# Performance work log

Hardware: AMD Instinct MI355X
Metric: run time of the kernel (lower is better)

The kernel has to match this reference:

```python
import jax, jax.numpy as jnp
import numpy as np

BATCH = 4096
NUM_FEATURES = 2048
DEPTH = 4
KERNEL = 2
THRESHOLD = 0.0


def setup_inputs() -> dict:
    key = jax.random.key(0)
    keys = jax.random.split(key, 2 + 2 * DEPTH + 2)
    inp = {}
    inp['x'] = jax.random.normal(keys[0], (BATCH, NUM_FEATURES), dtype=jnp.float32)
    # Conv2d(1,1,kernel_size=2) weight (k,k) and scalar bias, PyTorch-style init scale
    fan_in = KERNEL * KERNEL
    bound = 1.0 / np.sqrt(fan_in)
    inp['conv_w'] = jax.random.uniform(keys[1], (KERNEL, KERNEL), jnp.float32, -bound, bound)
    inp['conv_b'] = jax.random.uniform(keys[2], (), jnp.float32, -bound, bound)
    # MLP hidden layers
    lb = 1.0 / np.sqrt(NUM_FEATURES)
    for i in range(DEPTH):
        inp[f'W{i}'] = jax.random.uniform(keys[3 + 2 * i], (NUM_FEATURES, NUM_FEATURES), jnp.float32, -lb, lb)
        inp[f'b{i}'] = jax.random.uniform(keys[4 + 2 * i], (NUM_FEATURES,), jnp.float32, -lb, lb)
    inp['Wh'] = jax.random.uniform(keys[3 + 2 * DEPTH], (2, NUM_FEATURES), jnp.float32, -lb, lb)
    inp['bh'] = jax.random.uniform(keys[4 + 2 * DEPTH], (2,), jnp.float32, -lb, lb)
    return inp


def reference(x, conv_w, conv_b, W0, b0, W1, b1, W2, b2, W3, b3, Wh, bh):
    # Per-feature ConvFilter on a constant k x k patch of value x_i collapses to
    # sigmoid(x_i * sum(conv_w) + conv_b - threshold)  -- one fused elementwise op.
    h = jax.nn.sigmoid(x * jnp.sum(conv_w) + conv_b - THRESHOLD)  # (B, F)
    for W, b in ((W0, b0), (W1, b1), (W2, b2), (W3, b3)):
        h = jax.nn.relu(h @ W.T + b)
    return h @ Wh.T + bh  # (B, 2)
```

## Files before the change

### kernel.cpp

```cpp
#include <hip/hip_runtime.h>
#include <math.h>

#define BATCH 4096
#define NF    2048

typedef signed char    i8;
typedef unsigned int   u32;
typedef __attribute__((ext_vector_type(4))) int   intx4;
typedef __attribute__((ext_vector_type(4))) float floatx4;

#define LBW 0.022097086912079612f
#define QMAX 32512.0f
#define AMAX_H 3.0f

__global__ __launch_bounds__(256) void prep_kernel(
    const float* __restrict__ x, const float* __restrict__ cw,
    const float* __restrict__ cb,
    const float* __restrict__ w0, const float* __restrict__ w1,
    const float* __restrict__ w2, const float* __restrict__ w3,
    i8* __restrict__ h1o, i8* __restrict__ h2o,
    i8* __restrict__ q1,  i8* __restrict__ q2)
{
    const int bid = blockIdx.x;
    if (bid < 8192) {
        const float s = cw[0] + cw[1] + cw[2] + cw[3];
        const float c = cb[0];
        const int i = bid * 256 + threadIdx.x;
        float4 v = ((const float4*)x)[i];
        float vv[4] = {v.x, v.y, v.z, v.w};
        char4 c1, c2;
        #pragma unroll
        for (int j = 0; j < 4; ++j) {
            float r = 1.0f / (1.0f + expf(-(vv[j] * s + c)));
            int X = (int)(r * QMAX + 0.5f);
            int h1 = (X + 128) >> 8;
            int h2 = X - (h1 << 8);
            ((i8*)&c1)[j] = (i8)h1;
            ((i8*)&c2)[j] = (i8)h2;
        }
        *(char4*)&h1o[(size_t)i * 4] = c1;
        *(char4*)&h2o[(size_t)i * 4] = c2;
    } else {
        const int b2    = bid - 8192;
        const int layer = b2 >> 12;
        const int i     = (b2 & 4095) * 256 + threadIdx.x;
        const float* w = (layer == 0) ? w0 : (layer == 1) ? w1
                       : (layer == 2) ? w2 : w3;
        const size_t base = (size_t)layer * (size_t)NF * NF;
        float4 v = ((const float4*)w)[i];
        float vv[4] = {v.x, v.y, v.z, v.w};
        char4 c1, c2;
        #pragma unroll
        for (int j = 0; j < 4; ++j) {
            int X = (int)floorf(vv[j] * (QMAX / LBW) + 0.5f);
            X = max(-32512, min(32512, X));
            int h1 = (X + 128) >> 8;
            int h2 = X - (h1 << 8);
            ((i8*)&c1)[j] = (i8)h1;
            ((i8*)&c2)[j] = (i8)h2;
        }
        *(char4*)&q1[base + (size_t)i * 4] = c1;
        *(char4*)&q2[base + (size_t)i * 4] = c2;
    }
}

#define BM 128
#define BN 128
#define BK 64

__device__ __forceinline__ void stage16(const void* g, void* l) {
    __builtin_amdgcn_global_load_lds(
        (const __attribute__((address_space(1))) u32*)g,
        (__attribute__((address_space(3))) u32*)l, 16, 0, 0);
}

__global__ __launch_bounds__(256, 2) void gemm_i8_split(
    const i8* __restrict__ A1, const i8* __restrict__ A2,
    const i8* __restrict__ B1, const i8* __restrict__ B2,
    const float* __restrict__ bias,
    i8* __restrict__ C1, i8* __restrict__ C2,
    const float* __restrict__ Wh, const float* __restrict__ bh,
    float* __restrict__ outp,
    float combo, float outscale, int last, int M, int N, int K)
{
    __shared__ i8 sA1[BM * BK];
    __shared__ i8 sA2[BM * BK];
    __shared__ i8 sB1[BN * BK];
    __shared__ i8 sB2[BN * BK];

    const int t    = threadIdx.x;
    const int wv   = t >> 6;
    const int ln   = t & 63;
    const int quad = ln >> 4;
    const int ml   = ln & 15;
    const int wm   = wv >> 1;
    const int wn   = wv & 1;
    const int bm   = blockIdx.y * BM;
    const int bn   = blockIdx.x * BN;

    const int c0 = wv * 2, c1i = wv * 2 + 1;
    int offA0 = (bm + c0 * 16 + ml) * K + quad * 16;
    int offA1 = (bm + c1i * 16 + ml) * K + quad * 16;
    int offB0 = (bn + c0 * 16 + ml) * K + quad * 16;
    int offB1 = (bn + c1i * 16 + ml) * K + quad * 16;

    intx4 zero = {0, 0, 0, 0};
    intx4 acc11[4][4], accX[4][4];
    #pragma unroll
    for (int i = 0; i < 4; ++i)
        #pragma unroll
        for (int j = 0; j < 4; ++j) { acc11[i][j] = zero; accX[i][j] = zero; }

    for (int k0 = 0; k0 < K; k0 += BK) {
        stage16(A1 + offA0, &sA1[c0 * 1024]);
        stage16(A1 + offA1, &sA1[c1i * 1024]);
        stage16(A2 + offA0, &sA2[c0 * 1024]);
        stage16(A2 + offA1, &sA2[c1i * 1024]);
        stage16(B1 + offB0, &sB1[c0 * 1024]);
        stage16(B1 + offB1, &sB1[c1i * 1024]);
        stage16(B2 + offB0, &sB2[c0 * 1024]);
        stage16(B2 + offB1, &sB2[c1i * 1024]);
        offA0 += BK; offA1 += BK; offB0 += BK; offB1 += BK;
        __syncthreads();

        intx4 a1[4], a2[4];
        #pragma unroll
        for (int i = 0; i < 4; ++i) {
            const int ca = (wm * 4 + i) * 1024 + quad * 256 + ml * 16;
            a1[i] = *(const intx4*)&sA1[ca];
            a2[i] = *(const intx4*)&sA2[ca];
        }
        #pragma unroll
        for (int j = 0; j < 4; ++j) {
            const int cb = (wn * 4 + j) * 1024 + quad * 256 + ml * 16;
            intx4 b1 = *(const intx4*)&sB1[cb];
            intx4 b2 = *(const intx4*)&sB2[cb];
            #pragma unroll
            for (int i = 0; i < 4; ++i) {
                acc11[i][j] = __builtin_amdgcn_mfma_i32_16x16x64_i8(a1[i], b1, acc11[i][j], 0, 0, 0);
                accX[i][j]  = __builtin_amdgcn_mfma_i32_16x16x64_i8(a1[i], b2, accX[i][j], 0, 0, 0);
                accX[i][j]  = __builtin_amdgcn_mfma_i32_16x16x64_i8(a2[i], b1, accX[i][j], 0, 0, 0);
            }
        }
        __syncthreads();
    }

    if (!last) {
        #pragma unroll
        for (int j = 0; j < 4; ++j) {
            const int n  = bn + wn * 64 + j * 16 + ml;
            const float bv = bias[n];
            #pragma unroll
            for (int i = 0; i < 4; ++i) {
                #pragma unroll
                for (int r = 0; r < 4; ++r) {
                    const int m = bm + wm * 64 + i * 16 + quad * 4 + r;
                    float v = fmaf(65536.0f, (float)acc11[i][j][r],
                                   256.0f * (float)accX[i][j][r]) * combo + bv;
                    v = fmaxf(v, 0.0f);
                    int X = (int)(fminf(v * outscale, QMAX) + 0.5f);
                    int h1 = (X + 128) >> 8;
                    int h2 = X - (h1 << 8);
                    C1[(size_t)m * N + n] = (i8)h1;
                    C2[(size_t)m * N + n] = (i8)h2;
                }
            }
        }
    } else {
        float wh0[4], wh1[4], bv[4];
        #pragma unroll
        for (int j = 0; j < 4; ++j) {
            const int n = bn + wn * 64 + j * 16 + ml;
            bv[j]  = bias[n];
            wh0[j] = Wh[n];
            wh1[j] = Wh[NF + n];
        }
        #pragma unroll
        for (int i = 0; i < 4; ++i) {
            #pragma unroll
            for (int r = 0; r < 4; ++r) {
                float s0 = 0.0f, s1 = 0.0f;
                #pragma unroll
                for (int j = 0; j < 4; ++j) {
                    float v = fmaf(65536.0f, (float)acc11[i][j][r],
                                   256.0f * (float)accX[i][j][r]) * combo + bv[j];
                    v = fmaxf(v, 0.0f);
                    s0 = fmaf(v, wh0[j], s0);
                    s1 = fmaf(v, wh1[j], s1);
                }
                #pragma unroll
                for (int off = 8; off > 0; off >>= 1) {
                    s0 += __shfl_xor(s0, off, 64);
                    s1 += __shfl_xor(s1, off, 64);
                }
                if (ml == 0) {
                    const int m = bm + wm * 64 + i * 16 + quad * 4 + r;
                    if (bn == 0 && wn == 0) { s0 += bh[0]; s1 += bh[1]; }
                    atomicAdd(&outp[(size_t)m * 2 + 0], s0);
                    atomicAdd(&outp[(size_t)m * 2 + 1], s1);
                }
            }
        }
    }
}

__global__ __launch_bounds__(256) void act_kernel_f32(
    const float* __restrict__ x, const float* __restrict__ conv_w,
    const float* __restrict__ conv_b, float* __restrict__ h, int n4)
{
    const float s = conv_w[0] + conv_w[1] + conv_w[2] + conv_w[3];
    const float c = conv_b[0];
    int i = blockIdx.x * blockDim.x + threadIdx.x;
    if (i < n4) {
        float4 v = ((const float4*)x)[i];
        float4 r;
        r.x = 1.0f / (1.0f + expf(-(v.x * s + c)));
        r.y = 1.0f / (1.0f + expf(-(v.y * s + c)));
        r.z = 1.0f / (1.0f + expf(-(v.z * s + c)));
        r.w = 1.0f / (1.0f + expf(-(v.w * s + c)));
        ((float4*)h)[i] = r;
    }
}

#define FBM 128
#define FBN 128
#define FBK 16
#define FPAD 4

__global__ __launch_bounds__(256) void gemm_bias_relu_f32(
    const float* __restrict__ A, const float* __restrict__ W,
    const float* __restrict__ bias, float* __restrict__ C,
    int M, int N, int K, int do_relu)
{
    __shared__ float As[FBK][FBM + FPAD];
    __shared__ float Bs[FBK][FBN + FPAD];
    const int t  = threadIdx.x;
    const int bm = blockIdx.y * FBM;
    const int bn = blockIdx.x * FBN;
    const int tn = (t & 15) * 8;
    const int tm = (t >> 4) * 8;
    const int r0 = t >> 2;
    const int kv = (t & 3) << 2;
    float acc[8][8] = {};
    for (int k0 = 0; k0 < K; k0 += FBK) {
        #pragma unroll
        for (int half = 0; half < 2; ++half) {
            const int row = r0 + half * 64;
            float4 av = *(const float4*)&A[(size_t)(bm + row) * K + k0 + kv];
            As[kv + 0][row] = av.x; As[kv + 1][row] = av.y;
            As[kv + 2][row] = av.z; As[kv + 3][row] = av.w;
            float4 bv = *(const float4*)&W[(size_t)(bn + row) * K + k0 + kv];
            Bs[kv + 0][row] = bv.x; Bs[kv + 1][row] = bv.y;
            Bs[kv + 2][row] = bv.z; Bs[kv + 3][row] = bv.w;
        }
        __syncthreads();
        #pragma unroll
        for (int kk = 0; kk < FBK; ++kk) {
            float a[8], b[8];
            *(float4*)&a[0] = *(const float4*)&As[kk][tm];
            *(float4*)&a[4] = *(const float4*)&As[kk][tm + 4];
            *(float4*)&b[0] = *(const float4*)&Bs[kk][tn];
            *(float4*)&b[4] = *(const float4*)&Bs[kk][tn + 4];
            #pragma unroll
            for (int i = 0; i < 8; ++i)
                #pragma unroll
                for (int j = 0; j < 8; ++j)
                    acc[i][j] = fmaf(a[i], b[j], acc[i][j]);
        }
        __syncthreads();
    }
    #pragma unroll
    for (int i = 0; i < 8; ++i) {
        const int row = bm + tm + i;
        #pragma unroll
        for (int j = 0; j < 8; j += 4) {
            float4 v;
            v.x = acc[i][j + 0] + bias[bn + tn + j + 0];
            v.y = acc[i][j + 1] + bias[bn + tn + j + 1];
            v.z = acc[i][j + 2] + bias[bn + tn + j + 2];
            v.w = acc[i][j + 3] + bias[bn + tn + j + 3];
            if (do_relu) {
                v.x = fmaxf(v.x, 0.0f); v.y = fmaxf(v.y, 0.0f);
                v.z = fmaxf(v.z, 0.0f); v.w = fmaxf(v.w, 0.0f);
            }
            *(float4*)&C[(size_t)row * N + bn + tn + j] = v;
        }
    }
}

__global__ __launch_bounds__(256) void head_kernel_f32(
    const float* __restrict__ h, const float* __restrict__ Wh,
    const float* __restrict__ bh, float* __restrict__ out)
{
    const int wave = threadIdx.x >> 6;
    const int lane = threadIdx.x & 63;
    const int row  = blockIdx.x * 4 + wave;
    const float* hr = h + (size_t)row * NF;
    float acc0 = 0.0f, acc1 = 0.0f;
    for (int k = lane * 4; k < NF; k += 256) {
        float4 v  = *(const float4*)&hr[k];
        float4 w0 = *(const float4*)&Wh[k];
        float4 w1 = *(const float4*)&Wh[NF + k];
        acc0 += v.x * w0.x + v.y * w0.y + v.z * w0.z + v.w * w0.w;
        acc1 += v.x * w1.x + v.y * w1.y + v.z * w1.z + v.w * w1.w;
    }
    #pragma unroll
    for (int off = 32; off > 0; off >>= 1) {
        acc0 += __shfl_down(acc0, off, 64);
        acc1 += __shfl_down(acc1, off, 64);
    }
    if (lane == 0) {
        out[row * 2 + 0] = acc0 + bh[0];
        out[row * 2 + 1] = acc1 + bh[1];
    }
}

extern "C" void kernel_launch(void* const* d_in, const int* in_sizes, int n_in,
                              void* d_out, int out_size, void* d_ws, size_t ws_size,
                              hipStream_t stream)
{
    const float* x      = (const float*)d_in[0];
    const float* conv_w = (const float*)d_in[1];
    const float* conv_b = (const float*)d_in[2];
    const float* Ws[4]  = {(const float*)d_in[3], (const float*)d_in[5],
                           (const float*)d_in[7], (const float*)d_in[9]};
    const float* bs[4]  = {(const float*)d_in[4], (const float*)d_in[6],
                           (const float*)d_in[8], (const float*)d_in[10]};
    const float* Wh     = (const float*)d_in[11];
    const float* bh     = (const float*)d_in[12];
    float* out = (float*)d_out;

    const size_t AE = (size_t)BATCH * NF;
    const size_t WE = (size_t)NF * NF;
    const size_t need_i8 = 4 * AE + 8 * WE;

    const int n4 = (BATCH * NF) / 4;

    if (ws_size >= need_i8) {
        i8* base = (i8*)d_ws;
        i8* a01 = base;
        i8* a02 = a01 + AE;
        i8* a11 = a02 + AE;
        i8* a12 = a11 + AE;
        i8* wq1 = a12 + AE;
        i8* wq2 = wq1 + 4 * WE;

        hipMemsetAsync(out, 0, (size_t)out_size * sizeof(float), stream);

        prep_kernel<<<8192 + 16384, 256, 0, stream>>>(
            x, conv_w, conv_b, Ws[0], Ws[1], Ws[2], Ws[3],
            a01, a02, wq1, wq2);

        const float sW = LBW / QMAX;
        const float outscale = QMAX / AMAX_H;
        dim3 grid(NF / BN, BATCH / BM);

        i8 *in1 = a01, *in2 = a02, *o1 = a11, *o2 = a12;
        for (int l = 0; l < 4; ++l) {
            const float sA = ((l == 0) ? 1.0f : AMAX_H) / QMAX;
            gemm_i8_split<<<grid, 256, 0, stream>>>(
                in1, in2, wq1 + (size_t)l * WE, wq2 + (size_t)l * WE,
                bs[l], o1, o2, Wh, bh, out,
                sA * sW, outscale, (l == 3) ? 1 : 0, BATCH, NF, NF);
            i8* t1 = in1; i8* t2 = in2;
            in1 = o1; in2 = o2; o1 = t1; o2 = t2;
        }
    } else {
        float* ws0 = (float*)d_ws;
        float* ws1 = ws0 + AE;
        act_kernel_f32<<<(n4 + 255) / 256, 256, 0, stream>>>(x, conv_w, conv_b, ws0, n4);
        dim3 fgrid(NF / FBN, BATCH / FBM);
        gemm_bias_relu_f32<<<fgrid, 256, 0, stream>>>(ws0, Ws[0], bs[0], ws1, BATCH, NF, NF, 1);
        gemm_bias_relu_f32<<<fgrid, 256, 0, stream>>>(ws1, Ws[1], bs[1], ws0, BATCH, NF, NF, 1);
        gemm_bias_relu_f32<<<fgrid, 256, 0, stream>>>(ws0, Ws[2], bs[2], ws1, BATCH, NF, NF, 1);
        gemm_bias_relu_f32<<<fgrid, 256, 0, stream>>>(ws1, Ws[3], bs[3], ws0, BATCH, NF, NF, 1);
        head_kernel_f32<<<BATCH / 4, 256, 0, stream>>>(ws0, Wh, bh, out);
    }
}
```

Baseline: 412.7 us.

## Enlarge int8 GEMM tile to 256x128 with 8 waves and double-buffered LDS pipeline

The split int8 GEMM moves from 128x128 tiles on 256 threads to 256x128 tiles on 512 threads (8 waves in a 4x2 layout). It uses 96KB of dynamic LDS, double-buffered, so global-to-LDS loads for the next K tile overlap with MFMA work on the current one. The K loop is split into four phases with barriers, interleaved LDS fragment loads, and s_setprio raised around the MFMA bursts. The aim is to hide load latency and improve data reuse. In exchange it uses many barriers, higher LDS and register pressure, and the epilogue must match the new wave mapping.

```diff
diff --git a/kernel.cpp b/kernel.cpp
--- a/kernel.cpp
+++ b/kernel.cpp
@@ -64,7 +64,7 @@
     }
 }
 
-#define BM 128
+#define BM 256
 #define BN 128
 #define BK 64
 
@@ -74,7 +74,7 @@
         (__attribute__((address_space(3))) u32*)l, 16, 0, 0);
 }
 
-__global__ __launch_bounds__(256, 2) void gemm_i8_split(
+__global__ __launch_bounds__(512, 2) void gemm_i8_split(
     const i8* __restrict__ A1, const i8* __restrict__ A2,
     const i8* __restrict__ B1, const i8* __restrict__ B2,
     const float* __restrict__ bias,
@@ -83,10 +83,11 @@
     float* __restrict__ outp,
     float combo, float outscale, int last, int M, int N, int K)
 {
-    __shared__ i8 sA1[BM * BK];
-    __shared__ i8 sA2[BM * BK];
-    __shared__ i8 sB1[BN * BK];
-    __shared__ i8 sB2[BN * BK];
+    extern __shared__ i8 smem[];
+    i8* const sA1 = smem;
+    i8* const sA2 = smem + 32768;
+    i8* const sB1 = smem + 65536;
+    i8* const sB2 = smem + 81920;
 
     const int t    = threadIdx.x;
     const int wv   = t >> 6;
@@ -97,12 +98,11 @@
     const int wn   = wv & 1;
     const int bm   = blockIdx.y * BM;
     const int bn   = blockIdx.x * BN;
-
-    const int c0 = wv * 2, c1i = wv * 2 + 1;
-    int offA0 = (bm + c0 * 16 + ml) * K + quad * 16;
-    int offA1 = (bm + c1i * 16 + ml) * K + quad * 16;
-    int offB0 = (bn + c0 * 16 + ml) * K + quad * 16;
-    int offB1 = (bn + c1i * 16 + ml) * K + quad * 16;
+    const int lnoff = ln * 16;
+
+    int rA0 = (bm + (wv * 2 + 0) * 16 + ml) * K + quad * 16;
+    int rA1 = (bm + (wv * 2 + 1) * 16 + ml) * K + quad * 16;
+    int rB  = (bn +  wv * 16          + ml) * K + quad * 16;
 
     intx4 zero = {0, 0, 0, 0};
     intx4 acc11[4][4], accX[4][4];
@@ -111,39 +111,89 @@
         #pragma unroll
         for (int j = 0; j < 4; ++j) { acc11[i][j] = zero; accX[i][j] = zero; }
 
-    for (int k0 = 0; k0 < K; k0 += BK) {
-        stage16(A1 + offA0, &sA1[c0 * 1024]);
-        stage16(A1 + offA1, &sA1[c1i * 1024]);
-        stage16(A2 + offA0, &sA2[c0 * 1024]);
-        stage16(A2 + offA1, &sA2[c1i * 1024]);
-        stage16(B1 + offB0, &sB1[c0 * 1024]);
-        stage16(B1 + offB1, &sB1[c1i * 1024]);
-        stage16(B2 + offB0, &sB2[c0 * 1024]);
-        stage16(B2 + offB1, &sB2[c1i * 1024]);
-        offA0 += BK; offA1 += BK; offB0 += BK; offB1 += BK;
-        __syncthreads();
-
-        intx4 a1[4], a2[4];
-        #pragma unroll
-        for (int i = 0; i < 4; ++i) {
-            const int ca = (wm * 4 + i) * 1024 + quad * 256 + ml * 16;
-            a1[i] = *(const intx4*)&sA1[ca];
-            a2[i] = *(const intx4*)&sA2[ca];
-        }
-        #pragma unroll
-        for (int j = 0; j < 4; ++j) {
-            const int cb = (wn * 4 + j) * 1024 + quad * 256 + ml * 16;
-            intx4 b1 = *(const intx4*)&sB1[cb];
-            intx4 b2 = *(const intx4*)&sB2[cb];
-            #pragma unroll
-            for (int i = 0; i < 4; ++i) {
-                acc11[i][j] = __builtin_amdgcn_mfma_i32_16x16x64_i8(a1[i], b1, acc11[i][j], 0, 0, 0);
-                accX[i][j]  = __builtin_amdgcn_mfma_i32_16x16x64_i8(a1[i], b2, accX[i][j], 0, 0, 0);
-                accX[i][j]  = __builtin_amdgcn_mfma_i32_16x16x64_i8(a2[i], b1, accX[i][j], 0, 0, 0);
-            }
-        }
-        __syncthreads();
-    }
+    stage16(A1 + rA0, sA1 + (wv * 2 + 0) * 1024);
+    stage16(A1 + rA1, sA1 + (wv * 2 + 1) * 1024);
+    stage16(A2 + rA0, sA2 + (wv * 2 + 0) * 1024);
+    stage16(A2 + rA1, sA2 + (wv * 2 + 1) * 1024);
+    stage16(B1 + rB,  sB1 + wv * 1024);
+    stage16(B2 + rB,  sB2 + wv * 1024);
+    rA0 += BK; rA1 += BK; rB += BK;
+    asm volatile("s_waitcnt vmcnt(0)" ::: "memory");
+    __builtin_amdgcn_s_barrier();
+    asm volatile("" ::: "memory");
+
+    intx4 a1f0, a1f1, a2f0, a2f1;
+    intx4 b1lo0, b1lo1, b2lo0, b2lo1, b1hi0, b1hi1, b2hi0, b2hi1;
+
+#define LDA_(P, CUR, c) (*(const intx4*)&(P)[(CUR) * 16384 + (c) * 1024 + lnoff])
+#define LDB_(P, CUR, c) (*(const intx4*)&(P)[(CUR) * 8192  + (c) * 1024 + lnoff])
+#define MFMA3(i, j, A1R, A2R, B1R, B2R) \
+    acc11[i][j] = __builtin_amdgcn_mfma_i32_16x16x64_i8(A1R, B1R, acc11[i][j], 0, 0, 0); \
+    accX [i][j] = __builtin_amdgcn_mfma_i32_16x16x64_i8(A1R, B2R, accX [i][j], 0, 0, 0); \
+    accX [i][j] = __builtin_amdgcn_mfma_i32_16x16x64_i8(A2R, B1R, accX [i][j], 0, 0, 0);
+#define FENCE_   asm volatile("" ::: "memory")
+#define BARRIER_ FENCE_; __builtin_amdgcn_s_barrier(); FENCE_
+#define LGKM0_   asm volatile("s_waitcnt lgkmcnt(0)" ::: "memory")
+
+#define KTILE(CUR, SG) { \
+     \
+    a1f0 = LDA_(sA1, CUR, wm * 4 + 0);  a1f1 = LDA_(sA1, CUR, wm * 4 + 1); \
+    a2f0 = LDA_(sA2, CUR, wm * 4 + 0);  a2f1 = LDA_(sA2, CUR, wm * 4 + 1); \
+    b1lo0 = LDB_(sB1, CUR, wn * 4 + 0); b1lo1 = LDB_(sB1, CUR, wn * 4 + 1); \
+    b2lo0 = LDB_(sB2, CUR, wn * 4 + 0); b2lo1 = LDB_(sB2, CUR, wn * 4 + 1); \
+    if (SG) { stage16(A1 + rA0, sA1 + (1 - (CUR)) * 16384 + (wv * 2 + 0) * 1024); \
+              stage16(A1 + rA1, sA1 + (1 - (CUR)) * 16384 + (wv * 2 + 1) * 1024); } \
+    BARRIER_; LGKM0_; \
+    __builtin_amdgcn_s_setprio(1); \
+    MFMA3(0, 0, a1f0, a2f0, b1lo0, b2lo0) MFMA3(0, 1, a1f0, a2f0, b1lo1, b2lo1) \
+    MFMA3(1, 0, a1f1, a2f1, b1lo0, b2lo0) MFMA3(1, 1, a1f1, a2f1, b1lo1, b2lo1) \
+    __builtin_amdgcn_s_setprio(0); \
+    BARRIER_; \
+     \
+    b1hi0 = LDB_(sB1, CUR, wn * 4 + 2); b1hi1 = LDB_(sB1, CUR, wn * 4 + 3); \
+    b2hi0 = LDB_(sB2, CUR, wn * 4 + 2); b2hi1 = LDB_(sB2, CUR, wn * 4 + 3); \
+    if (SG) { stage16(A2 + rA0, sA2 + (1 - (CUR)) * 16384 + (wv * 2 + 0) * 1024); \
+              stage16(A2 + rA1, sA2 + (1 - (CUR)) * 16384 + (wv * 2 + 1) * 1024); } \
+    BARRIER_; LGKM0_; \
+    __builtin_amdgcn_s_setprio(1); \
+    MFMA3(0, 2, a1f0, a2f0, b1hi0, b2hi0) MFMA3(0, 3, a1f0, a2f0, b1hi1, b2hi1) \
+    MFMA3(1, 2, a1f1, a2f1, b1hi0, b2hi0) MFMA3(1, 3, a1f1, a2f1, b1hi1, b2hi1) \
+    __builtin_amdgcn_s_setprio(0); \
+    BARRIER_; \
+     \
+    a1f0 = LDA_(sA1, CUR, wm * 4 + 2);  a1f1 = LDA_(sA1, CUR, wm * 4 + 3); \
+    a2f0 = LDA_(sA2, CUR, wm * 4 + 2);  a2f1 = LDA_(sA2, CUR, wm * 4 + 3); \
+    if (SG) { stage16(B1 + rB, sB1 + (1 - (CUR)) * 8192 + wv * 1024); \
+              stage16(B2 + rB, sB2 + (1 - (CUR)) * 8192 + wv * 1024); } \
+    rA0 += BK; rA1 += BK; rB += BK; \
+    BARRIER_; LGKM0_; \
+    __builtin_amdgcn_s_setprio(1); \
+    MFMA3(2, 2, a1f0, a2f0, b1hi0, b2hi0) MFMA3(2, 3, a1f0, a2f0, b1hi1, b2hi1) \
+    MFMA3(3, 2, a1f1, a2f1, b1hi0, b2hi0) MFMA3(3, 3, a1f1, a2f1, b1hi1, b2hi1) \
+    __builtin_amdgcn_s_setprio(0); \
+     \
+    asm volatile("s_waitcnt vmcnt(0)" ::: "memory"); \
+    BARRIER_; \
+    __builtin_amdgcn_s_setprio(1); \
+    MFMA3(2, 0, a1f0, a2f0, b1lo0, b2lo0) MFMA3(2, 1, a1f0, a2f0, b1lo1, b2lo1) \
+    MFMA3(3, 0, a1f1, a2f1, b1lo0, b2lo0) MFMA3(3, 1, a1f1, a2f1, b1lo1, b2lo1) \
+    __builtin_amdgcn_s_setprio(0); \
+}
+
+    const int NIT = K >> 7;
+    #pragma unroll 1
+    for (int it = 0; it < NIT; ++it) {
+        KTILE(0, 1)
+        KTILE(1, (it < NIT - 1))
+    }
+
+#undef KTILE
+#undef LDA_
+#undef LDB_
+#undef MFMA3
+#undef FENCE_
+#undef BARRIER_
+#undef LGKM0_
 
     if (!last) {
         #pragma unroll
@@ -337,6 +387,14 @@
     const int n4 = (BATCH * NF) / 4;
 
     if (ws_size >= need_i8) {
+        static int attr_done = 0;
+        if (!attr_done) {
+            (void)hipFuncSetAttribute(
+                reinterpret_cast<const void*>(gemm_i8_split),
+                hipFuncAttributeMaxDynamicSharedMemorySize, 96 * 1024);
+            attr_done = 1;
+        }
+
         i8* base = (i8*)d_ws;
         i8* a01 = base;
         i8* a02 = a01 + AE;
@@ -358,7 +416,7 @@
         i8 *in1 = a01, *in2 = a02, *o1 = a11, *o2 = a12;
         for (int l = 0; l < 4; ++l) {
             const float sA = ((l == 0) ? 1.0f : AMAX_H) / QMAX;
-            gemm_i8_split<<<grid, 256, 0, stream>>>(
+            gemm_i8_split<<<grid, 512, 96 * 1024, stream>>>(
                 in1, in2, wq1 + (size_t)l * WE, wq2 + (size_t)l * WE,
                 bs[l], o1, o2, Wh, bh, out,
                 sA * sW, outscale, (l == 3) ? 1 : 0, BATCH, NF, NF);
```

Measured after the change: 404.3 us. 1.02x faster.
